# Optimization experiments

Hardware: AMD Instinct MI355X
Metric: run time of the kernel (lower is better)

## Reference

```python
import jax, jax.numpy as jnp
import numpy as np

B, T, D, P = 4096, 200, 64, 2
STEP_AHEAD_COV_REG = 1.0
THETA_DRIFT_REG = 0.1
GLOBAL_DIFF_REG = 0.01


def setup_inputs() -> dict:
    key = jax.random.key(0)
    k1, k2, k3, k4, k5, k6 = jax.random.split(key, 6)
    global_theta = jax.random.uniform(k1, (P,), dtype=jnp.float32) + 0.5  # keep away from 0 (divisor)
    pred_params = jax.random.normal(k2, (B, T, P), dtype=jnp.float32)
    hidden_states = jax.random.normal(k3, (B, T, D), dtype=jnp.float32)
    step_ahead_cov_preds = jax.random.normal(k4, (B, T - 1, D), dtype=jnp.float32)
    cov_trajs = jax.random.normal(k5, (B, T, D + 1), dtype=jnp.float32)
    lengths = jax.random.randint(k6, (B,), 1, T + 1, dtype=jnp.int32)
    return {
        "global_theta": global_theta,
        "pred_params": pred_params,
        "hidden_states": hidden_states,
        "step_ahead_cov_preds": step_ahead_cov_preds,
        "cov_trajs": cov_trajs,
        "lengths": lengths,
    }


def reference(global_theta, pred_params, hidden_states, step_ahead_cov_preds, cov_trajs, lengths):
    # --- step_ahead_cov_reg: masked per-individual mean of squared one-step-ahead error ---
    # original: mean over (length-1, D) of (cov_traj[1:length, 1:] - pred[0:length-1])**2 per individual
    diffs = (cov_trajs[:, 1:, 1:] - step_ahead_cov_preds) ** 2          # [B, T-1, D]
    t = jnp.arange(T - 1)
    mask = (t[None, :] < (lengths[:, None] - 1)).astype(diffs.dtype)    # [B, T-1]
    per_ind_sum = jnp.sum(diffs * mask[:, :, None], axis=(1, 2))        # [B]
    cnt = (jnp.maximum(lengths - 1, 1) * D).astype(diffs.dtype)
    per_ind = jnp.where(lengths > 1, per_ind_sum / cnt, 0.0)            # length==1 skipped -> 0
    step_ahead_cov_reg = jnp.mean(per_ind)

    # --- theta_drift_reg: mean squared consecutive-step difference of pred_params ---
    theta_drift_reg = jnp.mean((pred_params[:, :-1] - pred_params[:, 1:]) ** 2)

    # --- global_diff_reg: mean squared relative deviation from global_theta ---
    global_diff_reg = jnp.mean((pred_params / global_theta - 1.0) ** 2)

    return (STEP_AHEAD_COV_REG * step_ahead_cov_reg
            + THETA_DRIFT_REG * theta_drift_reg
            + GLOBAL_DIFF_REG * global_diff_reg)
```

## Files before the change

### kernel.cpp

```cpp
#include <hip/hip_runtime.h>

constexpr int Bn = 4096;
constexpr int Tn = 200;
constexpr int Dn = 64;
constexpr int Pn = 2;

constexpr int STEP_BLOCKS  = 4096;
constexpr int THETA_BLOCKS = 1024;
constexpr int N_PARTIALS   = STEP_BLOCKS + THETA_BLOCKS;

__device__ __forceinline__ float block_reduce(float v) {
#pragma unroll
    for (int off = 32; off > 0; off >>= 1)
        v += __shfl_down(v, off, 64);
    __shared__ float smem[8];
    const int lane = threadIdx.x & 63;
    const int wave = threadIdx.x >> 6;
    if (lane == 0) smem[wave] = v;
    __syncthreads();
    float s = 0.f;
    if (threadIdx.x == 0) {
        const int nw = (blockDim.x + 63) >> 6;
        for (int i = 0; i < nw; ++i) s += smem[i];
    }
    return s;
}

__global__ void step_kernel(const float* __restrict__ cov,
                            const float* __restrict__ preds,
                            const int* __restrict__ lengths,
                            float* __restrict__ partials) {
    constexpr unsigned QPB = (Tn - 1) * (Dn / 4);
    constexpr unsigned total = (unsigned)Bn * QPB;
    const float invBD = 1.0f / ((float)Dn * (float)Bn);
    float acc = 0.f;
    const unsigned stride = gridDim.x * blockDim.x;
    for (unsigned q = blockIdx.x * blockDim.x + threadIdx.x; q < total; q += stride) {
        const unsigned b = q / QPB;
        const unsigned r = q - b * QPB;
        const unsigned t = r >> 4;
        const unsigned d = (r & 15u) << 2;
        const int len = lengths[b];
        if ((int)t < len - 1) {
            const float4 p = *reinterpret_cast<const float4*>(
                preds + ((size_t)b * (Tn - 1) + t) * Dn + d);
            const float* c =
                cov + (size_t)b * Tn * (Dn + 1) + (size_t)(t + 1) * (Dn + 1) + 1 + d;
            const float d0 = c[0] - p.x;
            const float d1 = c[1] - p.y;
            const float d2 = c[2] - p.z;
            const float d3 = c[3] - p.w;
            acc += (d0 * d0 + d1 * d1 + d2 * d2 + d3 * d3) *
                   (invBD / (float)(len - 1));
        }
    }
    const float s = block_reduce(acc);
    if (threadIdx.x == 0) partials[blockIdx.x] = s;
}

__global__ void theta_kernel(const float* __restrict__ pp,
                             const float* __restrict__ theta,
                             float* __restrict__ partials) {
    const float r0 = 1.0f / theta[0];
    const float r1 = 1.0f / theta[1];
    const float gw = 0.01f / ((float)Bn * (float)Tn * (float)Pn);
    const float dw = 0.1f / ((float)Bn * (float)(Tn - 1) * (float)Pn);
    constexpr unsigned total = (unsigned)Bn * Tn;
    float acc = 0.f;
    const unsigned stride = gridDim.x * blockDim.x;
    for (unsigned i = blockIdx.x * blockDim.x + threadIdx.x; i < total; i += stride) {
        const unsigned t = i % Tn;
        const float2 x = *reinterpret_cast<const float2*>(pp + (size_t)i * 2);
        const float g0 = x.x * r0 - 1.0f;
        const float g1 = x.y * r1 - 1.0f;
        acc += (g0 * g0 + g1 * g1) * gw;
        if (t < Tn - 1) {
            const float2 y = *reinterpret_cast<const float2*>(pp + (size_t)i * 2 + 2);
            const float e0 = x.x - y.x;
            const float e1 = x.y - y.y;
            acc += (e0 * e0 + e1 * e1) * dw;
        }
    }
    const float s = block_reduce(acc);
    if (threadIdx.x == 0) partials[STEP_BLOCKS + blockIdx.x] = s;
}

__global__ void final_kernel(const float* __restrict__ partials,
                             float* __restrict__ out) {
    float acc = 0.f;
    for (int i = threadIdx.x; i < N_PARTIALS; i += blockDim.x)
        acc += partials[i];
    const float s = block_reduce(acc);
    if (threadIdx.x == 0) out[0] = s;
}

extern "C" void kernel_launch(void* const* d_in, const int* in_sizes, int n_in,
                              void* d_out, int out_size, void* d_ws, size_t ws_size,
                              hipStream_t stream) {
    const float* theta   = (const float*)d_in[0];
    const float* pp      = (const float*)d_in[1];
    const float* preds   = (const float*)d_in[3];
    const float* cov     = (const float*)d_in[4];
    const int*   lengths = (const int*)d_in[5];
    float* out      = (float*)d_out;
    float* partials = (float*)d_ws;

    step_kernel<<<STEP_BLOCKS, 256, 0, stream>>>(cov, preds, lengths, partials);
    theta_kernel<<<THETA_BLOCKS, 256, 0, stream>>>(pp, theta, partials);
    final_kernel<<<1, 256, 0, stream>>>(partials, out);
}
```

Baseline: 470.6 us.

## Fuse step and theta kernels, one block per individual with length-bounded loop

Merges the step-ahead and theta reduction kernels into one launch. Each of the first 4096 blocks now handles one individual and loops only over its valid timesteps, so the per-element division and mask test are gone and the per-individual scale is applied once. Theta work moves to 512 trailing blocks in the same grid. Pred loads use nontemporal hints. The price is load imbalance across blocks, since sequence lengths vary, and fewer theta blocks.

After: 460.4 us. -2.2%, faster.

```diff
diff --git a/kernel.cpp b/kernel.cpp
--- a/kernel.cpp
+++ b/kernel.cpp
@@ -5,84 +5,84 @@
 constexpr int Dn = 64;
 constexpr int Pn = 2;
 
-constexpr int STEP_BLOCKS  = 4096;
-constexpr int THETA_BLOCKS = 1024;
-constexpr int N_PARTIALS   = STEP_BLOCKS + THETA_BLOCKS;
+constexpr int THETA_BLOCKS = 512;
+constexpr int N_PARTIALS   = Bn + THETA_BLOCKS;
+
+typedef float f4 __attribute__((ext_vector_type(4)));
 
 __device__ __forceinline__ float block_reduce(float v) {
 #pragma unroll
     for (int off = 32; off > 0; off >>= 1)
         v += __shfl_down(v, off, 64);
-    __shared__ float smem[8];
+    __shared__ float smem[4];
     const int lane = threadIdx.x & 63;
     const int wave = threadIdx.x >> 6;
     if (lane == 0) smem[wave] = v;
     __syncthreads();
     float s = 0.f;
     if (threadIdx.x == 0) {
-        const int nw = (blockDim.x + 63) >> 6;
+        const int nw = blockDim.x >> 6;
         for (int i = 0; i < nw; ++i) s += smem[i];
     }
     return s;
 }
 
-__global__ void step_kernel(const float* __restrict__ cov,
-                            const float* __restrict__ preds,
-                            const int* __restrict__ lengths,
-                            float* __restrict__ partials) {
-    constexpr unsigned QPB = (Tn - 1) * (Dn / 4);
-    constexpr unsigned total = (unsigned)Bn * QPB;
-    const float invBD = 1.0f / ((float)Dn * (float)Bn);
-    float acc = 0.f;
-    const unsigned stride = gridDim.x * blockDim.x;
-    for (unsigned q = blockIdx.x * blockDim.x + threadIdx.x; q < total; q += stride) {
-        const unsigned b = q / QPB;
-        const unsigned r = q - b * QPB;
-        const unsigned t = r >> 4;
-        const unsigned d = (r & 15u) << 2;
+__global__ __launch_bounds__(256) void main_kernel(
+        const float* __restrict__ cov,
+        const float* __restrict__ preds,
+        const int*   __restrict__ lengths,
+        const float* __restrict__ pp,
+        const float* __restrict__ theta,
+        float*       __restrict__ partials) {
+    if (blockIdx.x < (unsigned)Bn) {
+        const int b   = blockIdx.x;
         const int len = lengths[b];
-        if ((int)t < len - 1) {
-            const float4 p = *reinterpret_cast<const float4*>(
-                preds + ((size_t)b * (Tn - 1) + t) * Dn + d);
-            const float* c =
-                cov + (size_t)b * Tn * (Dn + 1) + (size_t)(t + 1) * (Dn + 1) + 1 + d;
-            const float d0 = c[0] - p.x;
-            const float d1 = c[1] - p.y;
-            const float d2 = c[2] - p.z;
-            const float d3 = c[3] - p.w;
-            acc += (d0 * d0 + d1 * d1 + d2 * d2 + d3 * d3) *
-                   (invBD / (float)(len - 1));
+        float acc = 0.f;
+        if (len > 1) {
+            const unsigned nq = (unsigned)(len - 1) * (Dn / 4);
+            const float* __restrict__ pbase = preds + (size_t)b * (Tn - 1) * Dn;
+            const float* __restrict__ cbase = cov   + (size_t)b * Tn * (Dn + 1)
+                                              + (Dn + 1) + 1;
+            for (unsigned r = threadIdx.x; r < nq; r += 256) {
+                const unsigned t = r >> 4;
+                const unsigned d = (r & 15u) << 2;
+                const f4 p = __builtin_nontemporal_load(
+                    reinterpret_cast<const f4*>(pbase + (size_t)t * Dn + d));
+                const float* c = cbase + (size_t)t * (Dn + 1) + d;
+                const float d0 = c[0] - p.x;
+                const float d1 = c[1] - p.y;
+                const float d2 = c[2] - p.z;
+                const float d3 = c[3] - p.w;
+                acc += d0 * d0 + d1 * d1 + d2 * d2 + d3 * d3;
+            }
+            acc *= 1.0f / ((float)Dn * (float)Bn * (float)(len - 1));
         }
+        const float s = block_reduce(acc);
+        if (threadIdx.x == 0) partials[b] = s;
+    } else {
+        const float r0 = 1.0f / theta[0];
+        const float r1 = 1.0f / theta[1];
+        const float gw = 0.01f / ((float)Bn * (float)Tn * (float)Pn);
+        const float dw = 0.1f  / ((float)Bn * (float)(Tn - 1) * (float)Pn);
+        constexpr unsigned total = (unsigned)Bn * Tn;
+        float acc = 0.f;
+        const unsigned stride = THETA_BLOCKS * 256;
+        for (unsigned i = (blockIdx.x - Bn) * 256 + threadIdx.x; i < total; i += stride) {
+            const unsigned t = i % (unsigned)Tn;
+            const float2 x = *reinterpret_cast<const float2*>(pp + (size_t)i * 2);
+            const float g0 = x.x * r0 - 1.0f;
+            const float g1 = x.y * r1 - 1.0f;
+            acc += (g0 * g0 + g1 * g1) * gw;
+            if (t < Tn - 1) {
+                const float2 y = *reinterpret_cast<const float2*>(pp + (size_t)i * 2 + 2);
+                const float e0 = x.x - y.x;
+                const float e1 = x.y - y.y;
+                acc += (e0 * e0 + e1 * e1) * dw;
+            }
+        }
+        const float s = block_reduce(acc);
+        if (threadIdx.x == 0) partials[blockIdx.x] = s;
     }
-    const float s = block_reduce(acc);
-    if (threadIdx.x == 0) partials[blockIdx.x] = s;
-}
-
-__global__ void theta_kernel(const float* __restrict__ pp,
-                             const float* __restrict__ theta,
-                             float* __restrict__ partials) {
-    const float r0 = 1.0f / theta[0];
-    const float r1 = 1.0f / theta[1];
-    const float gw = 0.01f / ((float)Bn * (float)Tn * (float)Pn);
-    const float dw = 0.1f / ((float)Bn * (float)(Tn - 1) * (float)Pn);
-    constexpr unsigned total = (unsigned)Bn * Tn;
-    float acc = 0.f;
-    const unsigned stride = gridDim.x * blockDim.x;
-    for (unsigned i = blockIdx.x * blockDim.x + threadIdx.x; i < total; i += stride) {
-        const unsigned t = i % Tn;
-        const float2 x = *reinterpret_cast<const float2*>(pp + (size_t)i * 2);
-        const float g0 = x.x * r0 - 1.0f;
-        const float g1 = x.y * r1 - 1.0f;
-        acc += (g0 * g0 + g1 * g1) * gw;
-        if (t < Tn - 1) {
-            const float2 y = *reinterpret_cast<const float2*>(pp + (size_t)i * 2 + 2);
-            const float e0 = x.x - y.x;
-            const float e1 = x.y - y.y;
-            acc += (e0 * e0 + e1 * e1) * dw;
-        }
-    }
-    const float s = block_reduce(acc);
-    if (threadIdx.x == 0) partials[STEP_BLOCKS + blockIdx.x] = s;
 }
 
 __global__ void final_kernel(const float* __restrict__ partials,
@@ -105,7 +105,6 @@
     float* out      = (float*)d_out;
     float* partials = (float*)d_ws;
 
-    step_kernel<<<STEP_BLOCKS, 256, 0, stream>>>(cov, preds, lengths, partials);
-    theta_kernel<<<THETA_BLOCKS, 256, 0, stream>>>(pp, theta, partials);
+    main_kernel<<<Bn + THETA_BLOCKS, 256, 0, stream>>>(cov, preds, lengths, pp, theta, partials);
     final_kernel<<<1, 256, 0, stream>>>(partials, out);
 }
```
